# Kernel optimization log

Measured on AMD Instinct MI355X. Metric: run time of the kernel, lower is better.

Reference implementation:

```python
import jax, jax.numpy as jnp
import numpy as np

N = 50000        # num nodes
E = 800000       # num edges (before self loops)
IN = 256         # in_channels
H = 4            # heads
C = 32           # out_channels per head
NEG_SLOPE = 0.2


def _glorot(key, shape):
    fan = shape[-2] * (shape[-1] if len(shape) > 2 else 1) + shape[-1]
    # PyG glorot: uniform(-s, s) with s = sqrt(6 / (fan_in + fan_out))
    s = float(np.sqrt(6.0 / (shape[-2] + shape[-1])))
    return jax.random.uniform(key, shape, jnp.float32, -s, s)


def setup_inputs() -> dict:
    key = jax.random.key(0)
    k1, k2, k3, k4, k5 = jax.random.split(key, 5)
    x = jax.random.normal(k1, (N, IN), jnp.float32)
    src = jax.random.randint(k2, (E,), 0, N)
    dst = jax.random.randint(k3, (E,), 0, N)
    # guarantee no self loops (module removes them then re-adds exactly N loops)
    dst = jnp.where(dst == src, (dst + 1) % N, dst)
    edge_index = jnp.stack([src, dst]).astype(jnp.int32)
    weight = _glorot(k4, (IN, H * C))
    att = _glorot(k5, (1, H, 2 * C))
    bias = jnp.zeros((H * C,), jnp.float32)
    return {"x": x, "weight": weight, "att": att, "bias": bias,
            "edge_index": edge_index}


def reference(x, weight, att, bias, edge_index):
    n = x.shape[0]
    # linear projection -> [N, H, C]
    h = (x @ weight).reshape(n, H, C)
    # add self loops (input edge_index has none)
    loops = jnp.arange(n, dtype=edge_index.dtype)
    ei = jnp.concatenate([edge_index, jnp.stack([loops, loops])], axis=1)
    src, dst = ei[0], ei[1]          # flow source_to_target: j=src(row 0), i=dst(row 1)
    x_j = h[src]                     # [E', H, C] source features
    x_i = h[dst]                     # [E', H, C] target features
    wl = att[:, :, :C]               # applied to x_i (first half of concat)
    wr = att[:, :, C:]               # applied to x_j
    alpha = (x_i * wl).sum(-1) + (x_j * wr).sum(-1)   # [E', H]
    alpha = jax.nn.leaky_relu(alpha, NEG_SLOPE)
    # NOTE: module normalizes softmax over edge_index[0] (src) segments
    seg = src
    amax = jax.ops.segment_max(alpha, seg, num_segments=n)
    alpha = jnp.exp(alpha - amax[seg])
    denom = jax.ops.segment_sum(alpha, seg, num_segments=n)
    alpha = alpha / (denom[seg] + 1e-16)
    # weighted messages, aggregated at edge_index[i] = edge_index[1] (dst)
    msg = x_j * alpha[:, :, None]                     # [E', H, C]
    out = jax.ops.segment_sum(msg, dst, num_segments=n)  # [N, H, C]
    return out.reshape(n, H * C) + bias
```

## Files before the change

### kernel.cpp

```cpp
#include <hip/hip_runtime.h>
#include <hip/hip_fp16.h>
#include <math.h>


#define NH 4
#define CH 32
#define HC 128
#define IND 256
#define NEG_SLOPE 0.2f
#define CSH 8
#define NCB_MAX 256
#define CHUNK 4096
#define BCAP 6144

typedef __attribute__((ext_vector_type(8))) short bf16x8;
typedef __attribute__((ext_vector_type(16))) float f32x16;

__device__ __forceinline__ unsigned short f2bf(float f) {
    unsigned int u = __float_as_uint(f);
    unsigned int r = (u + 0x7FFFu + ((u >> 16) & 1u)) >> 16;
    return (unsigned short)r;
}
__device__ __forceinline__ float bf2f(unsigned short s) {
    return __uint_as_float(((unsigned int)s) << 16);
}

__global__ __launch_bounds__(256) void k_wprep(const float* __restrict__ W,
                                               unsigned short* __restrict__ WT_bf,
                                               int* __restrict__ gcurS,
                                               int* __restrict__ gcurD) {
    int t = blockIdx.x * 256 + threadIdx.x;
    if (blockIdx.x == 0) { gcurS[threadIdx.x] = 0; gcurD[threadIdx.x] = 0; }
    if (t < IND * HC) {
        int c = t >> 8;
        int k = t & 255;
        WT_bf[t] = f2bf(W[k * HC + c]);
    }
}

__global__ __launch_bounds__(256) void k_gs(const float* __restrict__ x,
                                            const unsigned short* __restrict__ WT_bf,
                                            const float* __restrict__ att,
                                            unsigned short* __restrict__ h_bf,
                                            float* __restrict__ al,
                                            float* __restrict__ ar,
                                            const int* __restrict__ ei,
                                            int* __restrict__ gcurS,
                                            int* __restrict__ gcurD,
                                            unsigned int* __restrict__ recS,
                                            unsigned int* __restrict__ recD,
                                            int E, int NE, int ncb, int nsb, int N) {
    __shared__ float cs[128 * 129];

    const int tid = threadIdx.x;

    if (blockIdx.x < nsb) {
        unsigned int* srt = (unsigned int*)cs;
        int* cnt  = (int*)(srt + CHUNK);
        int* off  = cnt + NCB_MAX;
        int* cur  = off + NCB_MAX;
        int* gpos = cur + NCB_MAX;
        int* sc   = gpos + NCB_MAX;

        const int t0 = blockIdx.x * CHUNK;
        const int m  = min(CHUNK, NE - t0);

        unsigned int myrec[CHUNK / 256];
        int nmy = 0;
        for (int i = tid; i < m; i += 256) {
            int t = t0 + i;
            int src, dst;
            if (t < E) { src = ei[t]; dst = ei[E + t]; }
            else       { src = dst = t - E; }
            myrec[nmy++] = (unsigned int)src | ((unsigned int)dst << 16);
        }

        for (int side = 0; side < 2; side++) {
            cnt[tid] = 0;
            __syncthreads();
            int mybkt[CHUNK / 256];
            for (int k = 0; k < nmy; k++) {
                unsigned int r = myrec[k];
                int node = side ? (int)(r >> 16) : (int)(r & 0xFFFFu);
                mybkt[k] = node >> CSH;
                atomicAdd(&cnt[mybkt[k]], 1);
            }
            __syncthreads();
            int v = cnt[tid];
            sc[tid] = v;
            __syncthreads();
            for (int o = 1; o < 256; o <<= 1) {
                int t = (tid >= o) ? sc[tid - o] : 0;
                __syncthreads();
                sc[tid] += t;
                __syncthreads();
            }
            off[tid] = sc[tid] - v;
            cur[tid] = sc[tid] - v;
            __syncthreads();
            for (int k = 0; k < nmy; k++) {
                int p = atomicAdd(&cur[mybkt[k]], 1);
                srt[p] = myrec[k];
            }
            __syncthreads();
            int* gcur = side ? gcurD : gcurS;
            if (tid < ncb) {
                int c = cnt[tid];
                gpos[tid] = c ? atomicAdd(&gcur[tid], c) : 0;
            }
            __syncthreads();
            unsigned int* recX = side ? recD : recS;
            for (int i = tid; i < m; i += 256) {
                unsigned int r = srt[i];
                int node = side ? (int)(r >> 16) : (int)(r & 0xFFFFu);
                int cb = node >> CSH;
                int p  = gpos[cb] + (i - off[cb]);
                if (p < BCAP)
                    recX[(size_t)cb * BCAP + p] = r;
            }
            __syncthreads();
        }
        return;
    }

    unsigned short* wsT = (unsigned short*)cs;

    const int row0 = (blockIdx.x - nsb) * 128;
    const int wave = tid >> 6;
    const int lane = tid & 63;
    const int n32  = lane & 31;
    const int half = lane >> 5;

    {
        int c  = tid >> 1;
        int kh = (tid & 1) * 128;
        const unsigned short* src = WT_bf + c * IND + kh;
        unsigned short* dst = wsT + c * 258 + kh;
#pragma unroll
        for (int j = 0; j < 128; j += 8)
            *(int4*)(dst + j) = *(const int4*)(src + j);
    }
    __syncthreads();

    const int row   = row0 + wave * 32 + n32;
    const bool valid = row < N;
    const float* xrow = x + (size_t)row * IND + half * 8;

    f32x16 acc[4];
#pragma unroll
    for (int t = 0; t < 4; t++)
#pragma unroll
        for (int r = 0; r < 16; r++) acc[t][r] = 0.0f;

#pragma unroll 4
    for (int s = 0; s < 16; s++) {
        float4 v0 = make_float4(0.f, 0.f, 0.f, 0.f);
        float4 v1 = v0;
        if (valid) {
            v0 = *(const float4*)(xrow + s * 16);
            v1 = *(const float4*)(xrow + s * 16 + 4);
        }
        bf16x8 a;
        a[0] = (short)f2bf(v0.x); a[1] = (short)f2bf(v0.y);
        a[2] = (short)f2bf(v0.z); a[3] = (short)f2bf(v0.w);
        a[4] = (short)f2bf(v1.x); a[5] = (short)f2bf(v1.y);
        a[6] = (short)f2bf(v1.z); a[7] = (short)f2bf(v1.w);
#pragma unroll
        for (int t = 0; t < 4; t++) {
            bf16x8 b = *(const bf16x8*)(wsT + (t * 32 + n32) * 258 + s * 16 + half * 8);
            acc[t] = __builtin_amdgcn_mfma_f32_32x32x16_bf16(a, b, acc[t], 0, 0, 0);
        }
    }
    __syncthreads();

#pragma unroll
    for (int t = 0; t < 4; t++)
#pragma unroll
        for (int r = 0; r < 16; r++) {
            int rl = wave * 32 + (r & 3) + 8 * (r >> 2) + 4 * half;
            cs[rl * 129 + t * 32 + n32] = acc[t][r];
        }
    __syncthreads();

    const int rl   = tid >> 1;
    const int chf  = tid & 1;
    const int orow = row0 + rl;
    if (orow < N) {
        const float* cr = cs + rl * 129 + chf * 64;
        unsigned short* hp = h_bf + (size_t)orow * HC + chf * 64;
#pragma unroll
        for (int c = 0; c < 64; c += 8) {
            ushort4 o0, o1;
            o0.x = f2bf(cr[c]);     o0.y = f2bf(cr[c + 1]);
            o0.z = f2bf(cr[c + 2]); o0.w = f2bf(cr[c + 3]);
            o1.x = f2bf(cr[c + 4]); o1.y = f2bf(cr[c + 5]);
            o1.z = f2bf(cr[c + 6]); o1.w = f2bf(cr[c + 7]);
            *(ushort4*)(hp + c) = o0;
            *(ushort4*)(hp + c + 4) = o1;
        }
        const int h0 = 2 * chf, h1 = 2 * chf + 1;
        const float* w0 = att + h0 * (2 * CH);
        const float* w1 = att + h1 * (2 * CH);
        float sl0 = 0.f, sr0 = 0.f, sl1 = 0.f, sr1 = 0.f;
#pragma unroll
        for (int c = 0; c < CH; c++) {
            float v0 = cr[c];
            float v1 = cr[CH + c];
            sl0 += v0 * w0[c];  sr0 += v0 * w0[CH + c];
            sl1 += v1 * w1[c];  sr1 += v1 * w1[CH + c];
        }
        al[orow * NH + h0] = sl0;  al[orow * NH + h1] = sl1;
        ar[orow * NH + h0] = sr0;  ar[orow * NH + h1] = sr1;
    }
}

__global__ __launch_bounds__(256) void k_bucket(const unsigned int* __restrict__ recS,
                                                const unsigned int* __restrict__ recD,
                                                const int* __restrict__ gcurS,
                                                const int* __restrict__ gcurD,
                                                const float* __restrict__ al,
                                                const float* __restrict__ ar,
                                                unsigned short* __restrict__ adjD,
                                                int* __restrict__ rowB,
                                                int* __restrict__ rowE,
                                                float* __restrict__ arw,
                                                int ncb, int N) {
    __shared__ int cnt[256], cur[256], sc[256];
    __shared__ float lsums[256 * NH];
    __shared__ float lar[256 * NH];
    const int tid = threadIdx.x;

    if (blockIdx.x < ncb) {
        const int cb = blockIdx.x;
        const int b0 = cb * BCAP;
        const int tot_rec = min(gcurD[cb], BCAP);

        cnt[tid] = 0;
        __syncthreads();
        for (int i = tid; i < tot_rec; i += 256) {
            unsigned int r = recD[b0 + i];
            atomicAdd(&cnt[(r >> 16) & 255], 1);
        }
        __syncthreads();
        int v = cnt[tid];
        sc[tid] = v;
        __syncthreads();
        for (int o = 1; o < 256; o <<= 1) {
            int t = (tid >= o) ? sc[tid - o] : 0;
            __syncthreads();
            sc[tid] += t;
            __syncthreads();
        }
        int ex = sc[tid] - v;
        int node_g = (cb << CSH) + tid;
        if (node_g < N) { rowB[node_g] = b0 + ex; rowE[node_g] = b0 + ex + v; }
        cur[tid] = ex;
        __syncthreads();
        for (int i = tid; i < tot_rec; i += 256) {
            unsigned int r = recD[b0 + i];
            int node = (int)(r >> 16) & 255;
            int p = atomicAdd(&cur[node], 1);
            adjD[b0 + p] = (unsigned short)(r & 0xFFFFu);
        }
    } else {
        const int cb = blockIdx.x - ncb;
        const int b0 = cb * BCAP;
        const int b1 = b0 + min(gcurS[cb], BCAP);
        const int node_g = (cb << CSH) + tid;

        float4 arv = make_float4(0.f, 0.f, 0.f, 0.f);
        if (node_g < N) arv = *(const float4*)(ar + (size_t)node_g * NH);
        *(float4*)(lar + tid * NH) = arv;
        *(float4*)(lsums + tid * NH) = make_float4(0.f, 0.f, 0.f, 0.f);
        __syncthreads();

        int i = b0 + tid;
        for (; i + 256 < b1; i += 512) {
            unsigned int r0 = recS[i];
            unsigned int r1 = recS[i + 256];
            int sl0 = (int)(r0 & 255u), dst0 = (int)(r0 >> 16);
            int sl1 = (int)(r1 & 255u), dst1 = (int)(r1 >> 16);
            float4 av0 = *(const float4*)(al + (size_t)dst0 * NH);
            float4 av1 = *(const float4*)(al + (size_t)dst1 * NH);
            const float* w0 = lar + sl0 * NH;
            const float* w1 = lar + sl1 * NH;
            float a0 = av0.x + w0[0], a1 = av0.y + w0[1];
            float a2 = av0.z + w0[2], a3 = av0.w + w0[3];
            float c0 = av1.x + w1[0], c1 = av1.y + w1[1];
            float c2 = av1.z + w1[2], c3 = av1.w + w1[3];
            a0 = (a0 > 0.f) ? a0 : NEG_SLOPE * a0;
            a1 = (a1 > 0.f) ? a1 : NEG_SLOPE * a1;
            a2 = (a2 > 0.f) ? a2 : NEG_SLOPE * a2;
            a3 = (a3 > 0.f) ? a3 : NEG_SLOPE * a3;
            c0 = (c0 > 0.f) ? c0 : NEG_SLOPE * c0;
            c1 = (c1 > 0.f) ? c1 : NEG_SLOPE * c1;
            c2 = (c2 > 0.f) ? c2 : NEG_SLOPE * c2;
            c3 = (c3 > 0.f) ? c3 : NEG_SLOPE * c3;
            float* s0 = lsums + sl0 * NH;
            float* s1 = lsums + sl1 * NH;
            atomicAdd(s0 + 0, __expf(a0));
            atomicAdd(s0 + 1, __expf(a1));
            atomicAdd(s0 + 2, __expf(a2));
            atomicAdd(s0 + 3, __expf(a3));
            atomicAdd(s1 + 0, __expf(c0));
            atomicAdd(s1 + 1, __expf(c1));
            atomicAdd(s1 + 2, __expf(c2));
            atomicAdd(s1 + 3, __expf(c3));
        }
        if (i < b1) {
            unsigned int r = recS[i];
            int slot = (int)(r & 255u);
            int dst  = (int)(r >> 16);
            float4 alv = *(const float4*)(al + (size_t)dst * NH);
            const float* av = lar + slot * NH;
            float a0 = alv.x + av[0], a1 = alv.y + av[1];
            float a2 = alv.z + av[2], a3 = alv.w + av[3];
            a0 = (a0 > 0.f) ? a0 : NEG_SLOPE * a0;
            a1 = (a1 > 0.f) ? a1 : NEG_SLOPE * a1;
            a2 = (a2 > 0.f) ? a2 : NEG_SLOPE * a2;
            a3 = (a3 > 0.f) ? a3 : NEG_SLOPE * a3;
            float* sp = lsums + slot * NH;
            atomicAdd(sp + 0, __expf(a0));
            atomicAdd(sp + 1, __expf(a1));
            atomicAdd(sp + 2, __expf(a2));
            atomicAdd(sp + 3, __expf(a3));
        }
        __syncthreads();

        if (node_g < N) {
            const float* sp = lsums + tid * NH;
            float4 p0 = make_float4(arv.x, 1.0f / (sp[0] + 1e-16f),
                                    arv.y, 1.0f / (sp[1] + 1e-16f));
            float4 p1 = make_float4(arv.z, 1.0f / (sp[2] + 1e-16f),
                                    arv.w, 1.0f / (sp[3] + 1e-16f));
            *(float4*)(arw + (size_t)node_g * 8)     = p0;
            *(float4*)(arw + (size_t)node_g * 8 + 4) = p1;
        }
    }
}

__global__ __launch_bounds__(256) void k_agg(const int* __restrict__ rowB,
                                             const int* __restrict__ rowE,
                                             const unsigned short* __restrict__ adjD,
                                             const float* __restrict__ al,
                                             const float* __restrict__ arw,
                                             const unsigned short* __restrict__ h_bf,
                                             const float* __restrict__ bias,
                                             float* __restrict__ out, int N) {
    const int g = threadIdx.x >> 5;
    const int n = blockIdx.x * 8 + g;
    if (n >= N) return;
    const int l  = threadIdx.x & 31;
    const int c0 = l * 4;
    const int hh = l >> 3;
    const int beg = rowB[n], end = rowE[n];
    const float alv = al[n * NH + hh];

    float a0 = 0.f, a1 = 0.f, a2 = 0.f, a3 = 0.f;

    for (int base = beg; base < end; base += 32) {
        int idx = base + l;
        int av  = (idx < end) ? (int)adjD[idx] : 0;
        int cnt = min(32, end - base);
        int e = 0;
        for (; e + 4 <= cnt; e += 4) {
            int s0 = __shfl(av, e,     32);
            int s1 = __shfl(av, e + 1, 32);
            int s2 = __shfl(av, e + 2, 32);
            int s3 = __shfl(av, e + 3, 32);
            ushort4 u0 = *(const ushort4*)(h_bf + (size_t)s0 * HC + c0);
            ushort4 u1 = *(const ushort4*)(h_bf + (size_t)s1 * HC + c0);
            ushort4 u2 = *(const ushort4*)(h_bf + (size_t)s2 * HC + c0);
            ushort4 u3 = *(const ushort4*)(h_bf + (size_t)s3 * HC + c0);
            float2 p0 = *(const float2*)(arw + (size_t)s0 * 8 + hh * 2);
            float2 p1 = *(const float2*)(arw + (size_t)s1 * 8 + hh * 2);
            float2 p2 = *(const float2*)(arw + (size_t)s2 * 8 + hh * 2);
            float2 p3 = *(const float2*)(arw + (size_t)s3 * 8 + hh * 2);
            float t0 = alv + p0.x; t0 = (t0 > 0.f) ? t0 : NEG_SLOPE * t0;
            float t1 = alv + p1.x; t1 = (t1 > 0.f) ? t1 : NEG_SLOPE * t1;
            float t2 = alv + p2.x; t2 = (t2 > 0.f) ? t2 : NEG_SLOPE * t2;
            float t3 = alv + p3.x; t3 = (t3 > 0.f) ? t3 : NEG_SLOPE * t3;
            float w0 = __expf(t0) * p0.y;
            float w1 = __expf(t1) * p1.y;
            float w2 = __expf(t2) * p2.y;
            float w3 = __expf(t3) * p3.y;
            a0 += bf2f(u0.x) * w0; a1 += bf2f(u0.y) * w0;
            a2 += bf2f(u0.z) * w0; a3 += bf2f(u0.w) * w0;
            a0 += bf2f(u1.x) * w1; a1 += bf2f(u1.y) * w1;
            a2 += bf2f(u1.z) * w1; a3 += bf2f(u1.w) * w1;
            a0 += bf2f(u2.x) * w2; a1 += bf2f(u2.y) * w2;
            a2 += bf2f(u2.z) * w2; a3 += bf2f(u2.w) * w2;
            a0 += bf2f(u3.x) * w3; a1 += bf2f(u3.y) * w3;
            a2 += bf2f(u3.z) * w3; a3 += bf2f(u3.w) * w3;
        }
        for (; e < cnt; e++) {
            int s0 = __shfl(av, e, 32);
            ushort4 u0 = *(const ushort4*)(h_bf + (size_t)s0 * HC + c0);
            float2 p0 = *(const float2*)(arw + (size_t)s0 * 8 + hh * 2);
            float t0 = alv + p0.x; t0 = (t0 > 0.f) ? t0 : NEG_SLOPE * t0;
            float w0 = __expf(t0) * p0.y;
            a0 += bf2f(u0.x) * w0; a1 += bf2f(u0.y) * w0;
            a2 += bf2f(u0.z) * w0; a3 += bf2f(u0.w) * w0;
        }
    }
    float4 b4 = *(const float4*)(bias + c0);
    *(float4*)(out + (size_t)n * HC + c0) =
        make_float4(a0 + b4.x, a1 + b4.y, a2 + b4.z, a3 + b4.w);
}

extern "C" void kernel_launch(void* const* d_in, const int* in_sizes, int n_in,
                              void* d_out, int out_size, void* d_ws, size_t ws_size,
                              hipStream_t stream) {
    const float* x    = (const float*)d_in[0];
    const float* W    = (const float*)d_in[1];
    const float* att  = (const float*)d_in[2];
    const float* bias = (const float*)d_in[3];
    const int*   ei   = (const int*)d_in[4];

    const int N  = in_sizes[0] / IND;
    const int E  = in_sizes[4] / 2;
    const int NE = E + N;
    const int ncb = (N + (1 << CSH) - 1) >> CSH;
    const int nsb = (NE + CHUNK - 1) / CHUNK;
    const int ngb = (N + 127) / 128;
    float* out = (float*)d_out;
    const int nodeTot = N * NH;
    const size_t capTot = (size_t)ncb * BCAP;

    unsigned short* h_bf  = (unsigned short*)d_ws;
    unsigned short* WT_bf = h_bf + (size_t)N * HC;
    float* al   = (float*)(WT_bf + IND * HC);
    float* ar   = al + nodeTot;
    float* arw  = ar + nodeTot;
    unsigned int* recS = (unsigned int*)(arw + (size_t)N * 8);
    unsigned int* recD = recS + capTot;
    unsigned short* adjD = (unsigned short*)(recD + capTot);
    int* rowB    = (int*)(adjD + capTot + (capTot & 1));
    int* rowE    = rowB + N;
    int* gcurS   = rowE + N;
    int* gcurD   = gcurS + NCB_MAX;

    k_wprep<<<(IND * HC + 255) / 256, 256, 0, stream>>>(W, WT_bf, gcurS, gcurD);
    k_gs<<<nsb + ngb, 256, 0, stream>>>(x, WT_bf, att, h_bf, al, ar, ei,
                                        gcurS, gcurD, recS, recD,
                                        E, NE, ncb, nsb, N);
    k_bucket<<<2 * ncb, 256, 0, stream>>>(recS, recD, gcurS, gcurD, al, ar,
                                          adjD, rowB, rowE, arw, ncb, N);
    k_agg<<<(N + 7) / 8, 256, 0, stream>>>(rowB, rowE, adjD, al, arw, h_bf,
                                           bias, out, N);
}
```

Measured before the change: 206.9 us.

## Store projected features head-major and split aggregation per head for cache locality

The projection kernel now runs 512-thread blocks covering 256 rows, writing h in a head-major layout [H][N][32] in two staged passes through shared memory. The aggregation kernel assigns each block a single head, with 8 lanes per node, so the gathered table per block is a quarter of the feature matrix. This is meant to improve L2 hit rates on the random neighbour gathers. In exchange, each node's edge list and attention values are read four times, and a gather now fetches only 64 bytes per neighbour.

```diff
diff --git a/kernel.cpp b/kernel.cpp
--- a/kernel.cpp
+++ b/kernel.cpp
@@ -38,7 +38,7 @@
     }
 }
 
-__global__ __launch_bounds__(256) void k_gs(const float* __restrict__ x,
+__global__ __launch_bounds__(512) void k_gs(const float* __restrict__ x,
                                             const unsigned short* __restrict__ WT_bf,
                                             const float* __restrict__ att,
                                             unsigned short* __restrict__ h_bf,
@@ -50,7 +50,7 @@
                                             unsigned int* __restrict__ recS,
                                             unsigned int* __restrict__ recD,
                                             int E, int NE, int ncb, int nsb, int N) {
-    __shared__ float cs[128 * 129];
+    __shared__ float cs[128 * 132];
 
     const int tid = threadIdx.x;
 
@@ -65,9 +65,9 @@
         const int t0 = blockIdx.x * CHUNK;
         const int m  = min(CHUNK, NE - t0);
 
-        unsigned int myrec[CHUNK / 256];
+        unsigned int myrec[CHUNK / 512];
         int nmy = 0;
-        for (int i = tid; i < m; i += 256) {
+        for (int i = tid; i < m; i += 512) {
             int t = t0 + i;
             int src, dst;
             if (t < E) { src = ei[t]; dst = ei[E + t]; }
@@ -76,9 +76,9 @@
         }
 
         for (int side = 0; side < 2; side++) {
-            cnt[tid] = 0;
-            __syncthreads();
-            int mybkt[CHUNK / 256];
+            if (tid < 256) cnt[tid] = 0;
+            __syncthreads();
+            int mybkt[CHUNK / 512];
             for (int k = 0; k < nmy; k++) {
                 unsigned int r = myrec[k];
                 int node = side ? (int)(r >> 16) : (int)(r & 0xFFFFu);
@@ -86,17 +86,16 @@
                 atomicAdd(&cnt[mybkt[k]], 1);
             }
             __syncthreads();
-            int v = cnt[tid];
-            sc[tid] = v;
+            int v = (tid < 256) ? cnt[tid] : 0;
+            if (tid < 256) sc[tid] = v;
             __syncthreads();
             for (int o = 1; o < 256; o <<= 1) {
-                int t = (tid >= o) ? sc[tid - o] : 0;
+                int t = (tid >= o && tid < 256) ? sc[tid - o] : 0;
                 __syncthreads();
-                sc[tid] += t;
+                if (tid < 256) sc[tid] += t;
                 __syncthreads();
             }
-            off[tid] = sc[tid] - v;
-            cur[tid] = sc[tid] - v;
+            if (tid < 256) { off[tid] = sc[tid] - v; cur[tid] = sc[tid] - v; }
             __syncthreads();
             for (int k = 0; k < nmy; k++) {
                 int p = atomicAdd(&cur[mybkt[k]], 1);
@@ -110,7 +109,7 @@
             }
             __syncthreads();
             unsigned int* recX = side ? recD : recS;
-            for (int i = tid; i < m; i += 256) {
+            for (int i = tid; i < m; i += 512) {
                 unsigned int r = srt[i];
                 int node = side ? (int)(r >> 16) : (int)(r & 0xFFFFu);
                 int cb = node >> CSH;
@@ -125,19 +124,19 @@
 
     unsigned short* wsT = (unsigned short*)cs;
 
-    const int row0 = (blockIdx.x - nsb) * 128;
+    const int row0 = (blockIdx.x - nsb) * 256;
     const int wave = tid >> 6;
     const int lane = tid & 63;
     const int n32  = lane & 31;
     const int half = lane >> 5;
 
     {
-        int c  = tid >> 1;
-        int kh = (tid & 1) * 128;
-        const unsigned short* src = WT_bf + c * IND + kh;
-        unsigned short* dst = wsT + c * 258 + kh;
-#pragma unroll
-        for (int j = 0; j < 128; j += 8)
+        int c  = tid >> 2;
+        int kq = (tid & 3) * 64;
+        const unsigned short* src = WT_bf + c * IND + kq;
+        unsigned short* dst = wsT + c * 258 + kq;
+#pragma unroll
+        for (int j = 0; j < 64; j += 8)
             *(int4*)(dst + j) = *(const int4*)(src + j);
     }
     __syncthreads();
@@ -173,44 +172,48 @@
     }
     __syncthreads();
 
-#pragma unroll
-    for (int t = 0; t < 4; t++)
-#pragma unroll
-        for (int r = 0; r < 16; r++) {
-            int rl = wave * 32 + (r & 3) + 8 * (r >> 2) + 4 * half;
-            cs[rl * 129 + t * 32 + n32] = acc[t][r];
-        }
-    __syncthreads();
-
-    const int rl   = tid >> 1;
-    const int chf  = tid & 1;
-    const int orow = row0 + rl;
-    if (orow < N) {
-        const float* cr = cs + rl * 129 + chf * 64;
-        unsigned short* hp = h_bf + (size_t)orow * HC + chf * 64;
-#pragma unroll
-        for (int c = 0; c < 64; c += 8) {
-            ushort4 o0, o1;
-            o0.x = f2bf(cr[c]);     o0.y = f2bf(cr[c + 1]);
-            o0.z = f2bf(cr[c + 2]); o0.w = f2bf(cr[c + 3]);
-            o1.x = f2bf(cr[c + 4]); o1.y = f2bf(cr[c + 5]);
-            o1.z = f2bf(cr[c + 6]); o1.w = f2bf(cr[c + 7]);
-            *(ushort4*)(hp + c) = o0;
-            *(ushort4*)(hp + c + 4) = o1;
-        }
-        const int h0 = 2 * chf, h1 = 2 * chf + 1;
-        const float* w0 = att + h0 * (2 * CH);
-        const float* w1 = att + h1 * (2 * CH);
-        float sl0 = 0.f, sr0 = 0.f, sl1 = 0.f, sr1 = 0.f;
-#pragma unroll
-        for (int c = 0; c < CH; c++) {
-            float v0 = cr[c];
-            float v1 = cr[CH + c];
-            sl0 += v0 * w0[c];  sr0 += v0 * w0[CH + c];
-            sl1 += v1 * w1[c];  sr1 += v1 * w1[CH + c];
-        }
-        al[orow * NH + h0] = sl0;  al[orow * NH + h1] = sl1;
-        ar[orow * NH + h0] = sr0;  ar[orow * NH + h1] = sr1;
+    const size_t NT = (size_t)N * 32;
+    for (int pass = 0; pass < 2; pass++) {
+        if ((wave >> 2) == pass) {
+            const int lw = wave & 3;
+#pragma unroll
+            for (int t = 0; t < 4; t++)
+#pragma unroll
+                for (int r = 0; r < 16; r++) {
+                    int rl = lw * 32 + (r & 3) + 8 * (r >> 2) + 4 * half;
+                    cs[rl * 132 + t * 33 + n32] = acc[t][r];
+                }
+        }
+        __syncthreads();
+
+        const int rl   = tid >> 2;
+        const int hq   = tid & 3;
+        const int orow = row0 + pass * 128 + rl;
+        if (orow < N) {
+            const float* cr = cs + rl * 132 + hq * 33;
+            unsigned short* hp = h_bf + (size_t)hq * NT + (size_t)orow * 32;
+#pragma unroll
+            for (int c = 0; c < 32; c += 8) {
+                ushort4 o0, o1;
+                o0.x = f2bf(cr[c]);     o0.y = f2bf(cr[c + 1]);
+                o0.z = f2bf(cr[c + 2]); o0.w = f2bf(cr[c + 3]);
+                o1.x = f2bf(cr[c + 4]); o1.y = f2bf(cr[c + 5]);
+                o1.z = f2bf(cr[c + 6]); o1.w = f2bf(cr[c + 7]);
+                *(ushort4*)(hp + c) = o0;
+                *(ushort4*)(hp + c + 4) = o1;
+            }
+            const float* w0 = att + hq * (2 * CH);
+            float sl = 0.f, sr = 0.f;
+#pragma unroll
+            for (int c = 0; c < CH; c++) {
+                float v = cr[c];
+                sl += v * w0[c];
+                sr += v * w0[CH + c];
+            }
+            al[orow * NH + hq] = sl;
+            ar[orow * NH + hq] = sr;
+        }
+        __syncthreads();
     }
 }
 
@@ -347,62 +350,52 @@
                                              const unsigned short* __restrict__ h_bf,
                                              const float* __restrict__ bias,
                                              float* __restrict__ out, int N) {
-    const int g = threadIdx.x >> 5;
-    const int n = blockIdx.x * 8 + g;
+    const int h     = blockIdx.x & 3;
+    const int p     = (blockIdx.x >> 2) & 1;
+    const int chunk = (blockIdx.x >> 3) * 2 + p;
+    const int n     = chunk * 32 + (threadIdx.x >> 3);
     if (n >= N) return;
-    const int l  = threadIdx.x & 31;
-    const int c0 = l * 4;
-    const int hh = l >> 3;
+    const int sl = threadIdx.x & 7;
+    const unsigned short* htab = h_bf + (size_t)h * N * 32;
     const int beg = rowB[n], end = rowE[n];
-    const float alv = al[n * NH + hh];
+    const float alh = al[n * NH + h];
 
     float a0 = 0.f, a1 = 0.f, a2 = 0.f, a3 = 0.f;
 
-    for (int base = beg; base < end; base += 32) {
-        int idx = base + l;
+    for (int base = beg; base < end; base += 8) {
+        int idx = base + sl;
         int av  = (idx < end) ? (int)adjD[idx] : 0;
-        int cnt = min(32, end - base);
+        int cnt = min(8, end - base);
         int e = 0;
-        for (; e + 4 <= cnt; e += 4) {
-            int s0 = __shfl(av, e,     32);
-            int s1 = __shfl(av, e + 1, 32);
-            int s2 = __shfl(av, e + 2, 32);
-            int s3 = __shfl(av, e + 3, 32);
-            ushort4 u0 = *(const ushort4*)(h_bf + (size_t)s0 * HC + c0);
-            ushort4 u1 = *(const ushort4*)(h_bf + (size_t)s1 * HC + c0);
-            ushort4 u2 = *(const ushort4*)(h_bf + (size_t)s2 * HC + c0);
-            ushort4 u3 = *(const ushort4*)(h_bf + (size_t)s3 * HC + c0);
-            float2 p0 = *(const float2*)(arw + (size_t)s0 * 8 + hh * 2);
-            float2 p1 = *(const float2*)(arw + (size_t)s1 * 8 + hh * 2);
-            float2 p2 = *(const float2*)(arw + (size_t)s2 * 8 + hh * 2);
-            float2 p3 = *(const float2*)(arw + (size_t)s3 * 8 + hh * 2);
-            float t0 = alv + p0.x; t0 = (t0 > 0.f) ? t0 : NEG_SLOPE * t0;
-            float t1 = alv + p1.x; t1 = (t1 > 0.f) ? t1 : NEG_SLOPE * t1;
-            float t2 = alv + p2.x; t2 = (t2 > 0.f) ? t2 : NEG_SLOPE * t2;
-            float t3 = alv + p3.x; t3 = (t3 > 0.f) ? t3 : NEG_SLOPE * t3;
+        for (; e + 2 <= cnt; e += 2) {
+            int s0 = __shfl(av, e,     8);
+            int s1 = __shfl(av, e + 1, 8);
+            ushort4 u0 = *(const ushort4*)(htab + (size_t)s0 * 32 + sl * 4);
+            ushort4 u1 = *(const ushort4*)(htab + (size_t)s1 * 32 + sl * 4);
+            float2 p0 = *(const float2*)(arw + (size_t)s0 * 8 + h * 2);
+            float2 p1 = *(const float2*)(arw + (size_t)s1 * 8 + h * 2);
+            float t0 = alh + p0.x; t0 = (t0 > 0.f) ? t0 : NEG_SLOPE * t0;
+            float t1 = alh + p1.x; t1 = (t1 > 0.f) ? t1 : NEG_SLOPE * t1;
             float w0 = __expf(t0) * p0.y;
             float w1 = __expf(t1) * p1.y;
-            float w2 = __expf(t2) * p2.y;
-            float w3 = __expf(t3) * p3.y;
-            a0 += bf2f(u0.x) * w0; a1 += bf2f(u0.y) * w0;
-            a2 += bf2f(u0.z) * w0; a3 += bf2f(u0.w) * w0;
-            a0 += bf2f(u1.x) * w1; a1 += bf2f(u1.y) * w1;
-            a2 += bf2f(u1.z) * w1; a3 += bf2f(u1.w) * w1;
-            a0 += bf2f(u2.x) * w2; a1 += bf2f(u2.y) * w2;
-            a2 += bf2f(u2.z) * w2; a3 += bf2f(u2.w) * w2;
-            a0 += bf2f(u3.x) * w3; a1 += bf2f(u3.y) * w3;
-            a2 += bf2f(u3.z) * w3; a3 += bf2f(u3.w) * w3;
-        }
-        for (; e < cnt; e++) {
-            int s0 = __shfl(av, e, 32);
-            ushort4 u0 = *(const ushort4*)(h_bf + (size_t)s0 * HC + c0);
-            float2 p0 = *(const float2*)(arw + (size_t)s0 * 8 + hh * 2);
-            float t0 = alv + p0.x; t0 = (t0 > 0.f) ? t0 : NEG_SLOPE * t0;
+            a0 += bf2f(u0.x) * w0 + bf2f(u1.x) * w1;
+            a1 += bf2f(u0.y) * w0 + bf2f(u1.y) * w1;
+            a2 += bf2f(u0.z) * w0 + bf2f(u1.z) * w1;
+            a3 += bf2f(u0.w) * w0 + bf2f(u1.w) * w1;
+        }
+        if (e < cnt) {
+            int s0 = __shfl(av, e, 8);
+            ushort4 u0 = *(const ushort4*)(htab + (size_t)s0 * 32 + sl * 4);
+            float2 p0 = *(const float2*)(arw + (size_t)s0 * 8 + h * 2);
+            float t0 = alh + p0.x; t0 = (t0 > 0.f) ? t0 : NEG_SLOPE * t0;
             float w0 = __expf(t0) * p0.y;
-            a0 += bf2f(u0.x) * w0; a1 += bf2f(u0.y) * w0;
-            a2 += bf2f(u0.z) * w0; a3 += bf2f(u0.w) * w0;
-        }
-    }
+            a0 += bf2f(u0.x) * w0;
+            a1 += bf2f(u0.y) * w0;
+            a2 += bf2f(u0.z) * w0;
+            a3 += bf2f(u0.w) * w0;
+        }
+    }
+    const int c0 = h * CH + sl * 4;
     float4 b4 = *(const float4*)(bias + c0);
     *(float4*)(out + (size_t)n * HC + c0) =
         make_float4(a0 + b4.x, a1 + b4.y, a2 + b4.z, a3 + b4.w);
@@ -422,7 +415,9 @@
     const int NE = E + N;
     const int ncb = (N + (1 << CSH) - 1) >> CSH;
     const int nsb = (NE + CHUNK - 1) / CHUNK;
-    const int ngb = (N + 127) / 128;
+    const int ngb = (N + 255) / 256;
+    const int nch = (N + 31) / 32;
+    const int nab = ((nch + 1) / 2) * 8;
     float* out = (float*)d_out;
     const int nodeTot = N * NH;
     const size_t capTot = (size_t)ncb * BCAP;
@@ -441,11 +436,11 @@
     int* gcurD   = gcurS + NCB_MAX;
 
     k_wprep<<<(IND * HC + 255) / 256, 256, 0, stream>>>(W, WT_bf, gcurS, gcurD);
-    k_gs<<<nsb + ngb, 256, 0, stream>>>(x, WT_bf, att, h_bf, al, ar, ei,
+    k_gs<<<nsb + ngb, 512, 0, stream>>>(x, WT_bf, att, h_bf, al, ar, ei,
                                         gcurS, gcurD, recS, recD,
                                         E, NE, ncb, nsb, N);
     k_bucket<<<2 * ncb, 256, 0, stream>>>(recS, recD, gcurS, gcurD, al, ar,
                                           adjD, rowB, rowE, arw, ncb, N);
-    k_agg<<<(N + 7) / 8, 256, 0, stream>>>(rowB, rowE, adjD, al, arw, h_bf,
-                                           bias, out, N);
-}
+    k_agg<<<nab, 256, 0, stream>>>(rowB, rowE, adjD, al, arw, h_bf,
+                                   bias, out, N);
+}
```

Result: slower. 218.8 us (+5.8%).
